# Optimization experiments

Measured on AMD Instinct MI355X. Metric: run time of the kernel, lower is better.

## Reference

```python
import jax, jax.numpy as jnp
import numpy as np

UNITS = 1024
N_CLASSES = 16
F_IN = 128
LN_EPS = 1e-3  # keras LayerNormalization default epsilon


def _lstm_cell(x, h, c, W, U, b):
    # keras LSTMCell gate order: i, f, g(candidate), o
    z = x @ W + h @ U + b  # [B, 4U]
    i, f, g, o = jnp.split(z, 4, axis=-1)
    i = jax.nn.sigmoid(i)
    f = jax.nn.sigmoid(f)
    g = jnp.tanh(g)
    o = jax.nn.sigmoid(o)
    c_new = f * c + i * g
    h_new = o * jnp.tanh(c_new)
    return h_new, c_new


def _layernorm(x, gamma, beta):
    mu = jnp.mean(x, axis=-1, keepdims=True)
    var = jnp.mean(jnp.square(x - mu), axis=-1, keepdims=True)
    return (x - mu) * jax.lax.rsqrt(var + LN_EPS) * gamma + beta


def setup_inputs() -> dict:
    key = jax.random.key(0)
    ks = jax.random.split(key, 8)
    s = 0.02
    inp = {
        "inputs": jax.random.normal(ks[0], (64, 512, F_IN), dtype=jnp.float32),
        "W0": jax.random.normal(ks[1], (F_IN, 4 * UNITS), dtype=jnp.float32) * s,
        "U0": jax.random.normal(ks[2], (UNITS, 4 * UNITS), dtype=jnp.float32) * s,
        "b0": jnp.zeros((4 * UNITS,), jnp.float32),
        "g0": jnp.ones((UNITS,), jnp.float32),
        "be0": jnp.zeros((UNITS,), jnp.float32),
        "W1": jax.random.normal(ks[3], (UNITS, 4 * UNITS), dtype=jnp.float32) * s,
        "U1": jax.random.normal(ks[4], (UNITS, 4 * UNITS), dtype=jnp.float32) * s,
        "b1": jnp.zeros((4 * UNITS,), jnp.float32),
        "g1": jnp.ones((UNITS,), jnp.float32),
        "be1": jnp.zeros((UNITS,), jnp.float32),
        "Wfc": jax.random.normal(ks[5], (UNITS, N_CLASSES), dtype=jnp.float32) * s,
        "bfc": jnp.zeros((N_CLASSES,), jnp.float32),
    }
    return inp


def reference(inputs, W0, U0, b0, g0, be0, W1, U1, b1, g1, be1, Wfc, bfc):
    B = inputs.shape[0]
    x_t = jnp.transpose(inputs, (1, 0, 2))  # [T, B, F]
    h0 = jnp.zeros((B, UNITS), jnp.float32)
    c0 = jnp.zeros((B, UNITS), jnp.float32)
    h1 = jnp.zeros((B, UNITS), jnp.float32)
    c1 = jnp.zeros((B, UNITS), jnp.float32)

    def step(carry, xt):
        h0, c0, h1, c1 = carry
        # layer 0: raw (h, c) carried across time; normalized output feeds layer 1
        h0n, c0n = _lstm_cell(xt, h0, c0, W0, U0, b0)
        o0 = _layernorm(h0n, g0, be0)
        h1n, c1n = _lstm_cell(o0, h1, c1, W1, U1, b1)
        o1 = _layernorm(h1n, g1, be1)
        # dropout is identity at inference (training=False)
        logits = jax.nn.softmax(o1 @ Wfc + bfc, axis=-1)
        return (h0n, c0n, h1n, c1n), logits

    _, out = jax.lax.scan(step, (h0, c0, h1, c1), x_t)  # [T, B, C]
    return jnp.transpose(out, (1, 0, 2))  # [B, T, C]
```

## Files before the change

### kernel.cpp

```cpp
#include <hip/hip_runtime.h>

typedef unsigned short u16;
typedef unsigned int u32;
typedef unsigned long long u64;
typedef __bf16 bf16x8 __attribute__((ext_vector_type(8)));
typedef float f32x4 __attribute__((ext_vector_type(4)));
typedef u32 u32x4 __attribute__((ext_vector_type(4)));

#define T_LEN 512
#define BATCH 64
#define FIN 128
#define UNITS 1024
#define H_STRIDE 65536

#define O_BAR   0
#define SZ_BAR  65536
#define O_XBF   SZ_BAR
#define SZ_XBF  (T_LEN*BATCH*FIN*2)
#define O_WP0   (O_XBF + SZ_XBF)
#define SZ_WP0  (1152*4096*2)
#define O_WP1   (O_WP0 + SZ_WP0)
#define SZ_WP1  (2048*4096*2)
#define O_WGFC  (O_WP1 + SZ_WP1)
#define SZ_WGFC (16384*2)
#define O_S1    (O_WGFC + SZ_WGFC)
#define SZ_S1   (4096*4)
#define O_B1C   (O_S1 + SZ_S1)
#define SZ_B1C  (4096*4)
#define O_SFC   (O_B1C + SZ_B1C)
#define SZ_SFC  64
#define O_BFCF  (O_SFC + SZ_SFC)
#define SZ_BFCF 64
#define O_H0    (O_BFCF + SZ_BFCF)
#define SZ_H    (2*H_STRIDE*2)
#define O_H1    (O_H0 + SZ_H)
#define WS_NEED (O_H1 + SZ_H)

__device__ __forceinline__ float bf2f(u16 s) {
  u32 u = ((u32)s) << 16;
  return __builtin_bit_cast(float, u);
}
__device__ __forceinline__ u16 f2bf(float f) {
  u32 u = __builtin_bit_cast(u32, f);
  u32 r = (u + 0x7FFFu + ((u >> 16) & 1u)) >> 16;
  return (u16)r;
}
__device__ __forceinline__ float sigm(float x) { return 1.0f / (1.0f + __expf(-x)); }
__device__ __forceinline__ float tanhft(float x) { return 1.0f - 2.0f / (__expf(2.0f * x) + 1.0f); }

__device__ __forceinline__ void sth(u16* q, u16 v) {
  __hip_atomic_store(q, v, __ATOMIC_RELAXED, __HIP_MEMORY_SCOPE_AGENT);
}

__device__ __forceinline__ void ldh2x64(const u16* qa, const u16* qb,
    u32x4& a0, u32x4& a1, u32x4& a2, u32x4& a3,
    u32x4& b0, u32x4& b1, u32x4& b2, u32x4& b3) {
  asm volatile(
    "global_load_dwordx4 %0, %8, off sc0 sc1\n\t"
    "global_load_dwordx4 %1, %8, off offset:512 sc0 sc1\n\t"
    "global_load_dwordx4 %2, %8, off offset:1024 sc0 sc1\n\t"
    "global_load_dwordx4 %3, %8, off offset:1536 sc0 sc1\n\t"
    "global_load_dwordx4 %4, %9, off sc0 sc1\n\t"
    "global_load_dwordx4 %5, %9, off offset:512 sc0 sc1\n\t"
    "global_load_dwordx4 %6, %9, off offset:1024 sc0 sc1\n\t"
    "global_load_dwordx4 %7, %9, off offset:1536 sc0 sc1\n\t"
    "s_waitcnt vmcnt(0)"
    : "=&v"(a0), "=&v"(a1), "=&v"(a2), "=&v"(a3),
      "=&v"(b0), "=&v"(b1), "=&v"(b2), "=&v"(b3)
    : "v"(qa), "v"(qb) : "memory");
}
__device__ __forceinline__ void ldh1x64(const u16* q,
    u32x4& a0, u32x4& a1, u32x4& a2, u32x4& a3) {
  asm volatile(
    "global_load_dwordx4 %0, %4, off sc0 sc1\n\t"
    "global_load_dwordx4 %1, %4, off offset:512 sc0 sc1\n\t"
    "global_load_dwordx4 %2, %4, off offset:1024 sc0 sc1\n\t"
    "global_load_dwordx4 %3, %4, off offset:1536 sc0 sc1\n\t"
    "s_waitcnt vmcnt(0)"
    : "=&v"(a0), "=&v"(a1), "=&v"(a2), "=&v"(a3)
    : "v"(q) : "memory");
}

__global__ void k_zero(u32* p, int n) {
  int i = blockIdx.x * 256 + threadIdx.x;
  if (i < n) p[i] = 0u;
}

__global__ void k_pack_x(const float* __restrict__ src, u16* __restrict__ dst) {
  int i = blockIdx.x * 256 + threadIdx.x;
  int f = i & 127, tb = i >> 7;
  int b = tb & 63, t = tb >> 6;
  dst[i] = f2bf(src[(b * T_LEN + t) * FIN + f]);
}

__global__ void k_pack_w0(const float* __restrict__ W0, const float* __restrict__ U0,
                          u16* __restrict__ dst) {
  int i = blockIdx.x * 256 + threadIdx.x;
  int j = i & 7, lane = (i >> 3) & 63, rest = i >> 9;
  int ktg = rest % 36, tmp = rest / 36;
  int nt = tmp & 3, ug = tmp >> 2;
  int k = ktg * 32 + ((lane >> 4) << 3) + j;
  int rr = nt * 16 + (lane & 15);
  int gate = rr & 3, ul = rr >> 2;
  int col = gate * 1024 + ug * 16 + ul;
  float v = (k < FIN) ? W0[k * 4096 + col] : U0[(k - FIN) * 4096 + col];
  dst[i] = f2bf(v);
}

__global__ void k_pack_w1(const float* __restrict__ W1, const float* __restrict__ U1,
                          const float* __restrict__ g0, u16* __restrict__ dst) {
  int i = blockIdx.x * 256 + threadIdx.x;
  int j = i & 7, lane = (i >> 3) & 63, rest = i >> 9;
  int ktg = rest & 63, tmp = rest >> 6;
  int nt = tmp & 3, ug = tmp >> 2;
  int k = ktg * 32 + ((lane >> 4) << 3) + j;
  int rr = nt * 16 + (lane & 15);
  int gate = rr & 3, ul = rr >> 2;
  int col = gate * 1024 + ug * 16 + ul;
  float v = (k < UNITS) ? g0[k] * W1[k * 4096 + col] : U1[(k - UNITS) * 4096 + col];
  dst[i] = f2bf(v);
}

__global__ void k_pack_s1(const float* __restrict__ W1, const float* __restrict__ g0,
                          const float* __restrict__ be0, const float* __restrict__ b1,
                          float* __restrict__ S1, float* __restrict__ B1C) {
  int n = blockIdx.x * 256 + threadIdx.x;
  float s = 0.f, c = 0.f;
  for (int k = 0; k < 1024; ++k) {
    float w = W1[k * 4096 + n];
    s += g0[k] * w;
    c += be0[k] * w;
  }
  S1[n] = s;
  B1C[n] = b1[n] + c;
}

__global__ void k_pack_wgfc(const float* __restrict__ Wfc, const float* __restrict__ g1,
                            u16* __restrict__ dst) {
  int i = blockIdx.x * 256 + threadIdx.x;
  int j = i & 7, lane = (i >> 3) & 63, s = i >> 9;
  int c = lane & 15;
  int k = s * 32 + ((lane >> 4) << 3) + j;
  dst[i] = f2bf(g1[k] * Wfc[k * 16 + c]);
}

__global__ void k_pack_sfc(const float* __restrict__ Wfc, const float* __restrict__ g1,
                           const float* __restrict__ be1, const float* __restrict__ bfc,
                           float* __restrict__ Sfc, float* __restrict__ Bf) {
  int c = threadIdx.x;
  if (c < 16) {
    float s = 0.f, b = 0.f;
    for (int k = 0; k < 1024; ++k) {
      float w = Wfc[k * 16 + c];
      s += g1[k] * w;
      b += be1[k] * w;
    }
    Sfc[c] = s;
    Bf[c] = bfc[c] + b;
  }
}

struct KP {
  const u16* xbf; const u16* wp0; const u16* wp1; const u16* wgfc;
  u16* h0; u16* h1; u32* bar;
  const float* b0; const float* s1; const float* b1c;
  const float* sfc; const float* bfcf;
  float* out;
};

__device__ __forceinline__ void accst4(u32x4 v, float& s1, float& s2) {
#pragma unroll
  for (int e = 0; e < 4; ++e) {
    float f0 = bf2f((u16)(v[e] & 0xffffu));
    float f1 = bf2f((u16)(v[e] >> 16));
    s1 += f0 + f1;
    s2 += f0 * f0 + f1 * f1;
  }
}

__device__ __forceinline__ void fc_wave0(int lane, int bg, int tout,
    const u16 (*bufB)[1032], const u16* wgB, const float* mu_s, const float* sg_s,
    float sfc_l, float bfc_l, float* __restrict__ out) {
  const int am = lane & 15, aq = (lane >> 4) << 3;
  f32x4 acc = {0.f, 0.f, 0.f, 0.f};
#pragma unroll
  for (int s = 0; s < 32; ++s) {
    bf16x8 a = *(const bf16x8*)&bufB[am][s * 32 + aq];
    bf16x8 b = *(const bf16x8*)&wgB[s * 512 + lane * 8];
    acc = __builtin_amdgcn_mfma_f32_16x16x32_bf16(a, b, acc, 0, 0, 0);
  }
  const int q = lane >> 4;
#pragma unroll
  for (int i = 0; i < 4; ++i) {
    int r = q * 4 + i;
    float rs = sg_s[r], mu = mu_s[r];
    float lg = rs * acc[i] - rs * mu * sfc_l + bfc_l;
    float mx = lg;
#pragma unroll
    for (int m = 1; m <= 8; m <<= 1) mx = fmaxf(mx, __shfl_xor(mx, m));
    float e = __expf(lg - mx), ss = e;
#pragma unroll
    for (int m = 1; m <= 8; m <<= 1) ss += __shfl_xor(ss, m);
    out[((size_t)(bg * 16 + r) * T_LEN + tout) * 16 + am] = e / ss;
  }
}

__global__ void __launch_bounds__(512, 2) k_persist(KP p) {
  const int tid = threadIdx.x;
  const int ug = blockIdx.x & 63, bg = blockIdx.x >> 6;
  const int lane = tid & 63, wv = tid >> 6;
  const int nt = wv & 3, kh = wv >> 2;

  __shared__ __align__(16) u16 bufA[16][1032];
  __shared__ __align__(16) u16 bufB[16][1032];
  __shared__ __align__(16) u16 wgB[16384];
  __shared__ float zb[2][16][68];
  __shared__ float b0s[64], b1s[64], S1b[64];
  __shared__ float al_s[16], be_s[16];
  __shared__ float mu_s[16], sg_s[16];

  if (tid < 64) {
    int gate = tid & 3, ul = tid >> 2;
    int col = gate * 1024 + ug * 16 + ul;
    b0s[tid] = p.b0[col];
    b1s[tid] = p.b1c[col];
    S1b[tid] = p.s1[col];
  }
  for (int i = tid * 8; i < 16384; i += 4096)
    *(uint4*)&wgB[i] = *(const uint4*)(p.wgfc + i);
  {
    u32* za = (u32*)&bufA[0][0];
    u32* zc = (u32*)&bufB[0][0];
    for (int i = tid; i < 16 * 1032 / 2; i += 512) { za[i] = 0u; zc[i] = 0u; }
  }
  const float sfc_l = p.sfc[lane & 15], bfc_l = p.bfcf[lane & 15];

  bf16x8 w0r[18], w1r[32];
  {
    const u16* q0 = p.wp0 + (size_t)(((ug * 4 + nt) * 36 + kh * 18) * 64 + lane) * 8;
#pragma unroll
    for (int s = 0; s < 18; ++s)
      w0r[s] = __builtin_bit_cast(bf16x8, *(const uint4*)(q0 + (size_t)s * 512));
    const u16* q1 = p.wp1 + (size_t)(((ug * 4 + nt) * 64 + kh * 32) * 64 + lane) * 8;
#pragma unroll
    for (int s = 0; s < 32; ++s)
      w1r[s] = __builtin_bit_cast(bf16x8, *(const uint4*)(q1 + (size_t)s * 512));
  }

  u32* flags = p.bar + bg * 2048;
  u32* gen   = p.bar + 8192 + bg * 32;

  float c0 = 0.f, c1 = 0.f;
  const int gr = tid >> 4, gu = tid & 15;
  const int srow = tid >> 5, ssub = tid & 31;
  const int am = lane & 15, aq = (lane >> 4) << 3;

  __syncthreads();

  for (int t = 0; t < T_LEN; ++t) {
    const int cur = t & 1, rd = cur ^ 1;

    f32x4 acc0 = {0.f, 0.f, 0.f, 0.f};
    if (kh == 0) {
      const u16* xr = p.xbf + (size_t)(t * 64 + bg * 16 + am) * FIN + aq;
#pragma unroll
      for (int s = 0; s < 4; ++s) {
        bf16x8 a = __builtin_bit_cast(bf16x8, *(const uint4*)(xr + s * 32));
        acc0 = __builtin_amdgcn_mfma_f32_16x16x32_bf16(a, w0r[s], acc0, 0, 0, 0);
      }
#pragma unroll
      for (int s = 4; s < 18; ++s) {
        bf16x8 a = __builtin_bit_cast(bf16x8, *(const uint4*)&bufA[am][s * 32 + aq - 128]);
        acc0 = __builtin_amdgcn_mfma_f32_16x16x32_bf16(a, w0r[s], acc0, 0, 0, 0);
      }
    } else {
#pragma unroll
      for (int s = 0; s < 18; ++s) {
        bf16x8 a = __builtin_bit_cast(bf16x8, *(const uint4*)&bufA[am][448 + s * 32 + aq]);
        acc0 = __builtin_amdgcn_mfma_f32_16x16x32_bf16(a, w0r[s], acc0, 0, 0, 0);
      }
    }
#pragma unroll
    for (int i = 0; i < 4; ++i)
      zb[kh][(lane >> 4) * 4 + i][nt * 16 + (lane & 15)] = acc0[i];
    __syncthreads();

    if (tid < 256) {
      const float* zr0 = &zb[0][gr][gu * 4];
      const float* zr1 = &zb[1][gr][gu * 4];
      float zi = zr0[0] + zr1[0] + b0s[gu * 4 + 0];
      float zf = zr0[1] + zr1[1] + b0s[gu * 4 + 1];
      float zg = zr0[2] + zr1[2] + b0s[gu * 4 + 2];
      float zo = zr0[3] + zr1[3] + b0s[gu * 4 + 3];
      float gi = sigm(zi), gf = sigm(zf), gg = tanhft(zg), go = sigm(zo);
      c0 = gf * c0 + gi * gg;
      float h = go * tanhft(c0);
      sth(p.h0 + (size_t)cur * H_STRIDE + (size_t)(bg * 16 + gr) * UNITS + ug * 16 + gu,
          f2bf(h));
    }
    __syncthreads();

    {
      const u32 ep = (u32)(t + 1);
      if (wv == 0) {
        if (lane == 0)
          __hip_atomic_store(flags + ug * 32, ep, __ATOMIC_RELAXED, __HIP_MEMORY_SCOPE_AGENT);
        if (ug == 63 && t >= 2)
          fc_wave0(lane, bg, t - 2, bufB, wgB, mu_s, sg_s, sfc_l, bfc_l, p.out);
        if (ug == 0) {
          for (;;) {
            u32 v = __hip_atomic_load(flags + lane * 32, __ATOMIC_RELAXED, __HIP_MEMORY_SCOPE_AGENT);
            if (__ballot(v >= ep) == ~0ull) break;
            __builtin_amdgcn_s_sleep(1);
          }
          if (lane == 0)
            __hip_atomic_store(gen, ep, __ATOMIC_RELAXED, __HIP_MEMORY_SCOPE_AGENT);
        } else {
          while (__hip_atomic_load(gen, __ATOMIC_RELAXED, __HIP_MEMORY_SCOPE_AGENT) < ep)
            __builtin_amdgcn_s_sleep(1);
        }
      }
      __syncthreads();
    }

    {
      const u16* h0r = p.h0 + (size_t)cur * H_STRIDE + (size_t)(bg * 16 + srow) * UNITS + ssub * 8;
      const u16* h1r = p.h1 + (size_t)rd  * H_STRIDE + (size_t)(bg * 16 + srow) * UNITS + ssub * 8;
      u32x4 a0, a1, a2, a3, b0, b1, b2, b3;
      ldh2x64(h0r, h1r, a0, a1, a2, a3, b0, b1, b2, b3);

      float s1 = 0.f, s2 = 0.f;
      accst4(a0, s1, s2); accst4(a1, s1, s2); accst4(a2, s1, s2); accst4(a3, s1, s2);
#pragma unroll
      for (int m = 1; m <= 16; m <<= 1) { s1 += __shfl_xor(s1, m); s2 += __shfl_xor(s2, m); }
      if (ssub == 0) {
        float mu = s1 * (1.0f / 1024.0f);
        float rs = rsqrtf(s2 * (1.0f / 1024.0f) - mu * mu + 1e-3f);
        al_s[srow] = rs;
        be_s[srow] = -rs * mu;
      }
      float u1 = 0.f, u2 = 0.f;
      accst4(b0, u1, u2); accst4(b1, u1, u2); accst4(b2, u1, u2); accst4(b3, u1, u2);
#pragma unroll
      for (int m = 1; m <= 16; m <<= 1) { u1 += __shfl_xor(u1, m); u2 += __shfl_xor(u2, m); }
      if (ssub == 0) {
        float mu = u1 * (1.0f / 1024.0f);
        mu_s[srow] = mu;
        sg_s[srow] = rsqrtf(u2 * (1.0f / 1024.0f) - mu * mu + 1e-3f);
      }
      *(u32x4*)&bufA[srow][ssub * 8]       = a0;
      *(u32x4*)&bufA[srow][256 + ssub * 8] = a1;
      *(u32x4*)&bufA[srow][512 + ssub * 8] = a2;
      *(u32x4*)&bufA[srow][768 + ssub * 8] = a3;
      *(u32x4*)&bufB[srow][ssub * 8]       = b0;
      *(u32x4*)&bufB[srow][256 + ssub * 8] = b1;
      *(u32x4*)&bufB[srow][512 + ssub * 8] = b2;
      *(u32x4*)&bufB[srow][768 + ssub * 8] = b3;
    }
    __syncthreads();

    f32x4 acc1 = {0.f, 0.f, 0.f, 0.f};
    if (kh == 0) {
#pragma unroll
      for (int s = 0; s < 32; ++s) {
        bf16x8 a = __builtin_bit_cast(bf16x8, *(const uint4*)&bufA[am][s * 32 + aq]);
        acc1 = __builtin_amdgcn_mfma_f32_16x16x32_bf16(a, w1r[s], acc1, 0, 0, 0);
      }
    } else {
#pragma unroll
      for (int s = 0; s < 32; ++s) {
        bf16x8 a = __builtin_bit_cast(bf16x8, *(const uint4*)&bufB[am][s * 32 + aq]);
        acc1 = __builtin_amdgcn_mfma_f32_16x16x32_bf16(a, w1r[s], acc1, 0, 0, 0);
      }
    }
#pragma unroll
    for (int i = 0; i < 4; ++i)
      zb[kh][(lane >> 4) * 4 + i][nt * 16 + (lane & 15)] = acc1[i];
    __syncthreads();

    if (tid < 256) {
      const float al = al_s[gr], be = be_s[gr];
      const float* zr0 = &zb[0][gr][gu * 4];
      const float* zr1 = &zb[1][gr][gu * 4];
      float zi = al * zr0[0] + be * S1b[gu * 4 + 0] + zr1[0] + b1s[gu * 4 + 0];
      float zf = al * zr0[1] + be * S1b[gu * 4 + 1] + zr1[1] + b1s[gu * 4 + 1];
      float zg = al * zr0[2] + be * S1b[gu * 4 + 2] + zr1[2] + b1s[gu * 4 + 2];
      float zo = al * zr0[3] + be * S1b[gu * 4 + 3] + zr1[3] + b1s[gu * 4 + 3];
      float gi = sigm(zi), gf = sigm(zf), gg = tanhft(zg), go = sigm(zo);
      c1 = gf * c1 + gi * gg;
      float h = go * tanhft(c1);
      sth(p.h1 + (size_t)cur * H_STRIDE + (size_t)(bg * 16 + gr) * UNITS + ug * 16 + gu,
          f2bf(h));
    }
    __syncthreads();
  }

  {
    const u32 ep = (u32)(T_LEN + 1);
    if (wv == 0) {
      if (lane == 0)
        __hip_atomic_store(flags + ug * 32, ep, __ATOMIC_RELAXED, __HIP_MEMORY_SCOPE_AGENT);
      if (ug == 63)
        fc_wave0(lane, bg, T_LEN - 2, bufB, wgB, mu_s, sg_s, sfc_l, bfc_l, p.out);
      if (ug == 0) {
        for (;;) {
          u32 v = __hip_atomic_load(flags + lane * 32, __ATOMIC_RELAXED, __HIP_MEMORY_SCOPE_AGENT);
          if (__ballot(v >= ep) == ~0ull) break;
          __builtin_amdgcn_s_sleep(1);
        }
        if (lane == 0)
          __hip_atomic_store(gen, ep, __ATOMIC_RELAXED, __HIP_MEMORY_SCOPE_AGENT);
      } else {
        while (__hip_atomic_load(gen, __ATOMIC_RELAXED, __HIP_MEMORY_SCOPE_AGENT) < ep)
          __builtin_amdgcn_s_sleep(1);
      }
    }
    __syncthreads();
  }
  {
    const u16* h1r = p.h1 + (size_t)((T_LEN - 1) & 1) * H_STRIDE
                   + (size_t)(bg * 16 + srow) * UNITS + ssub * 8;
    u32x4 b0, b1, b2, b3;
    ldh1x64(h1r, b0, b1, b2, b3);
    float u1 = 0.f, u2 = 0.f;
    accst4(b0, u1, u2); accst4(b1, u1, u2); accst4(b2, u1, u2); accst4(b3, u1, u2);
#pragma unroll
    for (int m = 1; m <= 16; m <<= 1) { u1 += __shfl_xor(u1, m); u2 += __shfl_xor(u2, m); }
    if (ssub == 0) {
      float mu = u1 * (1.0f / 1024.0f);
      mu_s[srow] = mu;
      sg_s[srow] = rsqrtf(u2 * (1.0f / 1024.0f) - mu * mu + 1e-3f);
    }
    *(u32x4*)&bufB[srow][ssub * 8]       = b0;
    *(u32x4*)&bufB[srow][256 + ssub * 8] = b1;
    *(u32x4*)&bufB[srow][512 + ssub * 8] = b2;
    *(u32x4*)&bufB[srow][768 + ssub * 8] = b3;
  }
  __syncthreads();
  if (ug == 63 && wv == 0)
    fc_wave0(lane, bg, T_LEN - 1, bufB, wgB, mu_s, sg_s, sfc_l, bfc_l, p.out);
}

extern "C" void kernel_launch(void* const* d_in, const int* in_sizes, int n_in,
                              void* d_out, int out_size, void* d_ws, size_t ws_size,
                              hipStream_t stream) {
  (void)in_sizes; (void)n_in; (void)out_size;
  if (ws_size < (size_t)WS_NEED) return;

  const float* inp = (const float*)d_in[0];
  const float* W0  = (const float*)d_in[1];
  const float* U0  = (const float*)d_in[2];
  const float* b0  = (const float*)d_in[3];
  const float* g0  = (const float*)d_in[4];
  const float* be0 = (const float*)d_in[5];
  const float* W1  = (const float*)d_in[6];
  const float* U1  = (const float*)d_in[7];
  const float* b1  = (const float*)d_in[8];
  const float* g1  = (const float*)d_in[9];
  const float* be1 = (const float*)d_in[10];
  const float* Wfc = (const float*)d_in[11];
  const float* bfc = (const float*)d_in[12];

  char* ws = (char*)d_ws;
  u32* bar  = (u32*)(ws + O_BAR);
  u16* xbf  = (u16*)(ws + O_XBF);
  u16* wp0  = (u16*)(ws + O_WP0);
  u16* wp1  = (u16*)(ws + O_WP1);
  u16* wgfc = (u16*)(ws + O_WGFC);
  float* S1   = (float*)(ws + O_S1);
  float* B1C  = (float*)(ws + O_B1C);
  float* Sfc  = (float*)(ws + O_SFC);
  float* Bf   = (float*)(ws + O_BFCF);
  u16* h0   = (u16*)(ws + O_H0);
  u16* h1   = (u16*)(ws + O_H1);

  k_zero<<<64, 256, 0, stream>>>(bar, 16384);
  k_zero<<<512, 256, 0, stream>>>((u32*)(ws + O_H0), (SZ_H + SZ_H) / 4);
  k_pack_x<<<16384, 256, 0, stream>>>(inp, xbf);
  k_pack_w0<<<18432, 256, 0, stream>>>(W0, U0, wp0);
  k_pack_w1<<<32768, 256, 0, stream>>>(W1, U1, g0, wp1);
  k_pack_s1<<<16, 256, 0, stream>>>(W1, g0, be0, b1, S1, B1C);
  k_pack_wgfc<<<64, 256, 0, stream>>>(Wfc, g1, wgfc);
  k_pack_sfc<<<1, 64, 0, stream>>>(Wfc, g1, be1, bfc, Sfc, Bf);

  KP p;
  p.xbf = xbf; p.wp0 = wp0; p.wp1 = wp1; p.wgfc = wgfc;
  p.h0 = h0; p.h1 = h1; p.bar = bar;
  p.b0 = b0; p.s1 = S1; p.b1c = B1C;
  p.sfc = Sfc; p.bfcf = Bf;
  p.out = (float*)d_out;

  void* args[] = { &p };
  hipLaunchCooperativeKernel((const void*)k_persist, dim3(256), dim3(512), args, 0, stream);
}
```

Before: 7.041 ms.

## Skew LSTM layers so layer-1 step t and layer-0 step t+1 share one grid barrier

Restructures the persistent kernel's time loop so layer 0 is computed one step ahead. Layer-1 step t and layer-0 step t+1 now run in the same phase after a single grid-wide barrier, where before each timestep had its own sequence of syncs and phases. This cuts the serialized barrier and sync phases per timestep roughly in half and lets the two MFMA chains and their gate activations overlap (threads 0-255 do layer 1, 256-511 do layer 0). It adds a prologue and epilogue, separate z buffers, and tricky ping-pong buffer indexing, which carries a correctness risk.

```diff
diff --git a/kernel.cpp b/kernel.cpp
--- a/kernel.cpp
+++ b/kernel.cpp
@@ -214,7 +214,8 @@
   __shared__ __align__(16) u16 bufA[16][1032];
   __shared__ __align__(16) u16 bufB[16][1032];
   __shared__ __align__(16) u16 wgB[16384];
-  __shared__ float zb[2][16][68];
+  __shared__ float zb0[2][16][68];
+  __shared__ float zb1[2][16][68];
   __shared__ float b0s[64], b1s[64], S1b[64];
   __shared__ float al_s[16], be_s[16];
   __shared__ float mu_s[16], sg_s[16];
@@ -230,8 +231,7 @@
     *(uint4*)&wgB[i] = *(const uint4*)(p.wgfc + i);
   {
     u32* za = (u32*)&bufA[0][0];
-    u32* zc = (u32*)&bufB[0][0];
-    for (int i = tid; i < 16 * 1032 / 2; i += 512) { za[i] = 0u; zc[i] = 0u; }
+    for (int i = tid; i < 16 * 1032 / 2; i += 512) za[i] = 0u;
   }
   const float sfc_l = p.sfc[lane & 15], bfc_l = p.bfcf[lane & 15];
 
@@ -251,18 +251,18 @@
   u32* gen   = p.bar + 8192 + bg * 32;
 
   float c0 = 0.f, c1 = 0.f;
-  const int gr = tid >> 4, gu = tid & 15;
+  const int gr = tid & 255 ? (tid & 255) >> 4 : 0;
+  const int grl = (tid & 255) >> 4, gul = tid & 15;
   const int srow = tid >> 5, ssub = tid & 31;
   const int am = lane & 15, aq = (lane >> 4) << 3;
+  (void)gr;
 
   __syncthreads();
 
-  for (int t = 0; t < T_LEN; ++t) {
-    const int cur = t & 1, rd = cur ^ 1;
-
+  {
     f32x4 acc0 = {0.f, 0.f, 0.f, 0.f};
     if (kh == 0) {
-      const u16* xr = p.xbf + (size_t)(t * 64 + bg * 16 + am) * FIN + aq;
+      const u16* xr = p.xbf + (size_t)(bg * 16 + am) * FIN + aq;
 #pragma unroll
       for (int s = 0; s < 4; ++s) {
         bf16x8 a = __builtin_bit_cast(bf16x8, *(const uint4*)(xr + s * 32));
@@ -282,46 +282,46 @@
     }
 #pragma unroll
     for (int i = 0; i < 4; ++i)
-      zb[kh][(lane >> 4) * 4 + i][nt * 16 + (lane & 15)] = acc0[i];
-    __syncthreads();
-
-    if (tid < 256) {
-      const float* zr0 = &zb[0][gr][gu * 4];
-      const float* zr1 = &zb[1][gr][gu * 4];
-      float zi = zr0[0] + zr1[0] + b0s[gu * 4 + 0];
-      float zf = zr0[1] + zr1[1] + b0s[gu * 4 + 1];
-      float zg = zr0[2] + zr1[2] + b0s[gu * 4 + 2];
-      float zo = zr0[3] + zr1[3] + b0s[gu * 4 + 3];
+      zb0[kh][(lane >> 4) * 4 + i][nt * 16 + (lane & 15)] = acc0[i];
+    __syncthreads();
+    if (tid >= 256) {
+      const float* zr0 = &zb0[0][grl][gul * 4];
+      const float* zr1 = &zb0[1][grl][gul * 4];
+      float zi = zr0[0] + zr1[0] + b0s[gul * 4 + 0];
+      float zf = zr0[1] + zr1[1] + b0s[gul * 4 + 1];
+      float zg = zr0[2] + zr1[2] + b0s[gul * 4 + 2];
+      float zo = zr0[3] + zr1[3] + b0s[gul * 4 + 3];
       float gi = sigm(zi), gf = sigm(zf), gg = tanhft(zg), go = sigm(zo);
       c0 = gf * c0 + gi * gg;
       float h = go * tanhft(c0);
-      sth(p.h0 + (size_t)cur * H_STRIDE + (size_t)(bg * 16 + gr) * UNITS + ug * 16 + gu,
-          f2bf(h));
-    }
-    __syncthreads();
-
-    {
-      const u32 ep = (u32)(t + 1);
-      if (wv == 0) {
+      sth(p.h0 + (size_t)(bg * 16 + grl) * UNITS + ug * 16 + gul, f2bf(h));
+    }
+    __syncthreads();
+  }
+
+  for (int t = 0; t < T_LEN - 1; ++t) {
+    const int cur = t & 1, rd = cur ^ 1;
+    const u32 ep = (u32)(t + 1);
+
+    if (wv == 0) {
+      if (lane == 0)
+        __hip_atomic_store(flags + ug * 32, ep, __ATOMIC_RELAXED, __HIP_MEMORY_SCOPE_AGENT);
+      if (ug == 63 && t >= 2)
+        fc_wave0(lane, bg, t - 2, bufB, wgB, mu_s, sg_s, sfc_l, bfc_l, p.out);
+      if (ug == 0) {
+        for (;;) {
+          u32 v = __hip_atomic_load(flags + lane * 32, __ATOMIC_RELAXED, __HIP_MEMORY_SCOPE_AGENT);
+          if (__ballot(v >= ep) == ~0ull) break;
+          __builtin_amdgcn_s_sleep(1);
+        }
         if (lane == 0)
-          __hip_atomic_store(flags + ug * 32, ep, __ATOMIC_RELAXED, __HIP_MEMORY_SCOPE_AGENT);
-        if (ug == 63 && t >= 2)
-          fc_wave0(lane, bg, t - 2, bufB, wgB, mu_s, sg_s, sfc_l, bfc_l, p.out);
-        if (ug == 0) {
-          for (;;) {
-            u32 v = __hip_atomic_load(flags + lane * 32, __ATOMIC_RELAXED, __HIP_MEMORY_SCOPE_AGENT);
-            if (__ballot(v >= ep) == ~0ull) break;
-            __builtin_amdgcn_s_sleep(1);
-          }
-          if (lane == 0)
-            __hip_atomic_store(gen, ep, __ATOMIC_RELAXED, __HIP_MEMORY_SCOPE_AGENT);
-        } else {
-          while (__hip_atomic_load(gen, __ATOMIC_RELAXED, __HIP_MEMORY_SCOPE_AGENT) < ep)
-            __builtin_amdgcn_s_sleep(1);
-        }
-      }
-      __syncthreads();
-    }
+          __hip_atomic_store(gen, ep, __ATOMIC_RELAXED, __HIP_MEMORY_SCOPE_AGENT);
+      } else {
+        while (__hip_atomic_load(gen, __ATOMIC_RELAXED, __HIP_MEMORY_SCOPE_AGENT) < ep)
+          __builtin_amdgcn_s_sleep(1);
+      }
+    }
+    __syncthreads();
 
     {
       const u16* h0r = p.h0 + (size_t)cur * H_STRIDE + (size_t)(bg * 16 + srow) * UNITS + ssub * 8;
@@ -359,6 +359,141 @@
     }
     __syncthreads();
 
+    {
+      bf16x8 xa[4];
+      if (kh == 0) {
+        const u16* xr = p.xbf + (size_t)((t + 1) * 64 + bg * 16 + am) * FIN + aq;
+#pragma unroll
+        for (int s = 0; s < 4; ++s)
+          xa[s] = __builtin_bit_cast(bf16x8, *(const uint4*)(xr + s * 32));
+      }
+      f32x4 acc1 = {0.f, 0.f, 0.f, 0.f};
+      if (kh == 0) {
+#pragma unroll
+        for (int s = 0; s < 32; ++s) {
+          bf16x8 a = __builtin_bit_cast(bf16x8, *(const uint4*)&bufA[am][s * 32 + aq]);
+          acc1 = __builtin_amdgcn_mfma_f32_16x16x32_bf16(a, w1r[s], acc1, 0, 0, 0);
+        }
+      } else {
+#pragma unroll
+        for (int s = 0; s < 32; ++s) {
+          bf16x8 a = __builtin_bit_cast(bf16x8, *(const uint4*)&bufB[am][s * 32 + aq]);
+          acc1 = __builtin_amdgcn_mfma_f32_16x16x32_bf16(a, w1r[s], acc1, 0, 0, 0);
+        }
+      }
+#pragma unroll
+      for (int i = 0; i < 4; ++i)
+        zb1[kh][(lane >> 4) * 4 + i][nt * 16 + (lane & 15)] = acc1[i];
+
+      f32x4 acc0 = {0.f, 0.f, 0.f, 0.f};
+      if (kh == 0) {
+#pragma unroll
+        for (int s = 0; s < 4; ++s)
+          acc0 = __builtin_amdgcn_mfma_f32_16x16x32_bf16(xa[s], w0r[s], acc0, 0, 0, 0);
+#pragma unroll
+        for (int s = 4; s < 18; ++s) {
+          bf16x8 a = __builtin_bit_cast(bf16x8, *(const uint4*)&bufA[am][s * 32 + aq - 128]);
+          acc0 = __builtin_amdgcn_mfma_f32_16x16x32_bf16(a, w0r[s], acc0, 0, 0, 0);
+        }
+      } else {
+#pragma unroll
+        for (int s = 0; s < 18; ++s) {
+          bf16x8 a = __builtin_bit_cast(bf16x8, *(const uint4*)&bufA[am][448 + s * 32 + aq]);
+          acc0 = __builtin_amdgcn_mfma_f32_16x16x32_bf16(a, w0r[s], acc0, 0, 0, 0);
+        }
+      }
+#pragma unroll
+      for (int i = 0; i < 4; ++i)
+        zb0[kh][(lane >> 4) * 4 + i][nt * 16 + (lane & 15)] = acc0[i];
+    }
+    __syncthreads();
+
+    if (tid < 256) {
+      const float al = al_s[grl], be = be_s[grl];
+      const float* zr0 = &zb1[0][grl][gul * 4];
+      const float* zr1 = &zb1[1][grl][gul * 4];
+      float zi = al * zr0[0] + be * S1b[gul * 4 + 0] + zr1[0] + b1s[gul * 4 + 0];
+      float zf = al * zr0[1] + be * S1b[gul * 4 + 1] + zr1[1] + b1s[gul * 4 + 1];
+      float zg = al * zr0[2] + be * S1b[gul * 4 + 2] + zr1[2] + b1s[gul * 4 + 2];
+      float zo = al * zr0[3] + be * S1b[gul * 4 + 3] + zr1[3] + b1s[gul * 4 + 3];
+      float gi = sigm(zi), gf = sigm(zf), gg = tanhft(zg), go = sigm(zo);
+      c1 = gf * c1 + gi * gg;
+      float h = go * tanhft(c1);
+      sth(p.h1 + (size_t)cur * H_STRIDE + (size_t)(bg * 16 + grl) * UNITS + ug * 16 + gul,
+          f2bf(h));
+    } else {
+      const float* zr0 = &zb0[0][grl][gul * 4];
+      const float* zr1 = &zb0[1][grl][gul * 4];
+      float zi = zr0[0] + zr1[0] + b0s[gul * 4 + 0];
+      float zf = zr0[1] + zr1[1] + b0s[gul * 4 + 1];
+      float zg = zr0[2] + zr1[2] + b0s[gul * 4 + 2];
+      float zo = zr0[3] + zr1[3] + b0s[gul * 4 + 3];
+      float gi = sigm(zi), gf = sigm(zf), gg = tanhft(zg), go = sigm(zo);
+      c0 = gf * c0 + gi * gg;
+      float h = go * tanhft(c0);
+      sth(p.h0 + (size_t)rd * H_STRIDE + (size_t)(bg * 16 + grl) * UNITS + ug * 16 + gul,
+          f2bf(h));
+    }
+    __syncthreads();
+  }
+
+  {
+    const u32 ep = (u32)T_LEN;
+    if (wv == 0) {
+      if (lane == 0)
+        __hip_atomic_store(flags + ug * 32, ep, __ATOMIC_RELAXED, __HIP_MEMORY_SCOPE_AGENT);
+      if (ug == 63)
+        fc_wave0(lane, bg, T_LEN - 3, bufB, wgB, mu_s, sg_s, sfc_l, bfc_l, p.out);
+      if (ug == 0) {
+        for (;;) {
+          u32 v = __hip_atomic_load(flags + lane * 32, __ATOMIC_RELAXED, __HIP_MEMORY_SCOPE_AGENT);
+          if (__ballot(v >= ep) == ~0ull) break;
+          __builtin_amdgcn_s_sleep(1);
+        }
+        if (lane == 0)
+          __hip_atomic_store(gen, ep, __ATOMIC_RELAXED, __HIP_MEMORY_SCOPE_AGENT);
+      } else {
+        while (__hip_atomic_load(gen, __ATOMIC_RELAXED, __HIP_MEMORY_SCOPE_AGENT) < ep)
+          __builtin_amdgcn_s_sleep(1);
+      }
+    }
+    __syncthreads();
+  }
+  {
+    const u16* h0r = p.h0 + (size_t)1 * H_STRIDE + (size_t)(bg * 16 + srow) * UNITS + ssub * 8;
+    const u16* h1r = p.h1 + (size_t)(bg * 16 + srow) * UNITS + ssub * 8;
+    u32x4 a0, a1, a2, a3, b0, b1, b2, b3;
+    ldh2x64(h0r, h1r, a0, a1, a2, a3, b0, b1, b2, b3);
+    float s1 = 0.f, s2 = 0.f;
+    accst4(a0, s1, s2); accst4(a1, s1, s2); accst4(a2, s1, s2); accst4(a3, s1, s2);
+#pragma unroll
+    for (int m = 1; m <= 16; m <<= 1) { s1 += __shfl_xor(s1, m); s2 += __shfl_xor(s2, m); }
+    if (ssub == 0) {
+      float mu = s1 * (1.0f / 1024.0f);
+      float rs = rsqrtf(s2 * (1.0f / 1024.0f) - mu * mu + 1e-3f);
+      al_s[srow] = rs;
+      be_s[srow] = -rs * mu;
+    }
+    float u1 = 0.f, u2 = 0.f;
+    accst4(b0, u1, u2); accst4(b1, u1, u2); accst4(b2, u1, u2); accst4(b3, u1, u2);
+#pragma unroll
+    for (int m = 1; m <= 16; m <<= 1) { u1 += __shfl_xor(u1, m); u2 += __shfl_xor(u2, m); }
+    if (ssub == 0) {
+      float mu = u1 * (1.0f / 1024.0f);
+      mu_s[srow] = mu;
+      sg_s[srow] = rsqrtf(u2 * (1.0f / 1024.0f) - mu * mu + 1e-3f);
+    }
+    *(u32x4*)&bufA[srow][ssub * 8]       = a0;
+    *(u32x4*)&bufA[srow][256 + ssub * 8] = a1;
+    *(u32x4*)&bufA[srow][512 + ssub * 8] = a2;
+    *(u32x4*)&bufA[srow][768 + ssub * 8] = a3;
+    *(u32x4*)&bufB[srow][ssub * 8]       = b0;
+    *(u32x4*)&bufB[srow][256 + ssub * 8] = b1;
+    *(u32x4*)&bufB[srow][512 + ssub * 8] = b2;
+    *(u32x4*)&bufB[srow][768 + ssub * 8] = b3;
+  }
+  __syncthreads();
+  {
     f32x4 acc1 = {0.f, 0.f, 0.f, 0.f};
     if (kh == 0) {
 #pragma unroll
@@ -375,25 +510,24 @@
     }
 #pragma unroll
     for (int i = 0; i < 4; ++i)
-      zb[kh][(lane >> 4) * 4 + i][nt * 16 + (lane & 15)] = acc1[i];
-    __syncthreads();
-
-    if (tid < 256) {
-      const float al = al_s[gr], be = be_s[gr];
-      const float* zr0 = &zb[0][gr][gu * 4];
-      const float* zr1 = &zb[1][gr][gu * 4];
-      float zi = al * zr0[0] + be * S1b[gu * 4 + 0] + zr1[0] + b1s[gu * 4 + 0];
-      float zf = al * zr0[1] + be * S1b[gu * 4 + 1] + zr1[1] + b1s[gu * 4 + 1];
-      float zg = al * zr0[2] + be * S1b[gu * 4 + 2] + zr1[2] + b1s[gu * 4 + 2];
-      float zo = al * zr0[3] + be * S1b[gu * 4 + 3] + zr1[3] + b1s[gu * 4 + 3];
-      float gi = sigm(zi), gf = sigm(zf), gg = tanhft(zg), go = sigm(zo);
-      c1 = gf * c1 + gi * gg;
-      float h = go * tanhft(c1);
-      sth(p.h1 + (size_t)cur * H_STRIDE + (size_t)(bg * 16 + gr) * UNITS + ug * 16 + gu,
-          f2bf(h));
-    }
-    __syncthreads();
-  }
+      zb1[kh][(lane >> 4) * 4 + i][nt * 16 + (lane & 15)] = acc1[i];
+  }
+  __syncthreads();
+  if (tid < 256) {
+    const float al = al_s[grl], be = be_s[grl];
+    const float* zr0 = &zb1[0][grl][gul * 4];
+    const float* zr1 = &zb1[1][grl][gul * 4];
+    float zi = al * zr0[0] + be * S1b[gul * 4 + 0] + zr1[0] + b1s[gul * 4 + 0];
+    float zf = al * zr0[1] + be * S1b[gul * 4 + 1] + zr1[1] + b1s[gul * 4 + 1];
+    float zg = al * zr0[2] + be * S1b[gul * 4 + 2] + zr1[2] + b1s[gul * 4 + 2];
+    float zo = al * zr0[3] + be * S1b[gul * 4 + 3] + zr1[3] + b1s[gul * 4 + 3];
+    float gi = sigm(zi), gf = sigm(zf), gg = tanhft(zg), go = sigm(zo);
+    c1 = gf * c1 + gi * gg;
+    float h = go * tanhft(c1);
+    sth(p.h1 + (size_t)1 * H_STRIDE + (size_t)(bg * 16 + grl) * UNITS + ug * 16 + gul,
+        f2bf(h));
+  }
+  __syncthreads();
 
   {
     const u32 ep = (u32)(T_LEN + 1);
@@ -410,16 +544,15 @@
         }
         if (lane == 0)
           __hip_atomic_store(gen, ep, __ATOMIC_RELAXED, __HIP_MEMORY_SCOPE_AGENT);
-      } else {
+      } else if (ug == 63) {
         while (__hip_atomic_load(gen, __ATOMIC_RELAXED, __HIP_MEMORY_SCOPE_AGENT) < ep)
           __builtin_amdgcn_s_sleep(1);
       }
     }
     __syncthreads();
   }
-  {
-    const u16* h1r = p.h1 + (size_t)((T_LEN - 1) & 1) * H_STRIDE
-                   + (size_t)(bg * 16 + srow) * UNITS + ssub * 8;
+  if (ug == 63) {
+    const u16* h1r = p.h1 + (size_t)1 * H_STRIDE + (size_t)(bg * 16 + srow) * UNITS + ssub * 8;
     u32x4 b0, b1, b2, b3;
     ldh1x64(h1r, b0, b1, b2, b3);
     float u1 = 0.f, u2 = 0.f;
@@ -435,10 +568,10 @@
     *(u32x4*)&bufB[srow][256 + ssub * 8] = b1;
     *(u32x4*)&bufB[srow][512 + ssub * 8] = b2;
     *(u32x4*)&bufB[srow][768 + ssub * 8] = b3;
-  }
-  __syncthreads();
-  if (ug == 63 && wv == 0)
-    fc_wave0(lane, bg, T_LEN - 1, bufB, wgB, mu_s, sg_s, sfc_l, bfc_l, p.out);
+    __syncthreads();
+    if (wv == 0)
+      fc_wave0(lane, bg, T_LEN - 1, bufB, wgB, mu_s, sg_s, sfc_l, bfc_l, p.out);
+  }
 }
 
 extern "C" void kernel_launch(void* const* d_in, const int* in_sizes, int n_in,
```

New measurement: 7.883 ms. 1.12x slower.
